# Kernel tuning notes

Measured on AMD Instinct MI355X. Metric: run time of the kernel, lower is better.

The kernel has to match this reference:

```python
import jax, jax.numpy as jnp
import numpy as np

B, NQ, NK, D, H = 2, 1024, 1024, 512, 32


def setup_inputs() -> dict:
    key = jax.random.key(0)
    ks = jax.random.split(key, 6)
    keys_t = jax.random.normal(ks[0], (B, NK, D), dtype=jnp.float32)
    queries = jax.random.normal(ks[1], (B, NQ, D), dtype=jnp.float32)
    # torch nn.Linear default init: U(-1/sqrt(fan_in), 1/sqrt(fan_in))
    s1 = 1.0 / np.sqrt(2 * D)
    W1 = jax.random.uniform(ks[2], (2 * D, H), jnp.float32, -s1, s1)  # (2d, hidden)
    b1 = jax.random.uniform(ks[3], (H,), jnp.float32, -s1, s1)
    s2 = 1.0 / np.sqrt(H)
    W2 = jax.random.uniform(ks[4], (H, 1), jnp.float32, -s2, s2)
    b2 = jax.random.uniform(ks[5], (1,), jnp.float32, -s2, s2)
    return {"keys": keys_t, "queries": queries, "W1": W1, "b1": b1, "W2": W2, "b2": b2}


def reference(keys, queries, W1, b1, W2, b2):
    # logits[b,q,k] = W2 . tanh(W1 @ cat(keys[b,k], queries[b,q]) + b1) + b2
    # Decompose first linear: cat(k,q) @ W1 == k @ W1[:D] + q @ W1[D:]
    d = keys.shape[-1]
    hk = jnp.einsum('bkd,dh->bkh', keys, W1[:d])      # (B, NK, H)
    hq = jnp.einsum('bqd,dh->bqh', queries, W1[d:])   # (B, NQ, H)
    h = jnp.tanh(hk[:, None, :, :] + hq[:, :, None, :] + b1)  # (B, NQ, NK, H)
    logits = jnp.einsum('bqkh,ho->bqko', h, W2)[..., 0] + b2[0]  # (B, NQ, NK)
    return logits
```

## Files before the change

kernel.cpp:

```cpp
#include <hip/hip_runtime.h>
#include <hip/hip_bf16.h>

#define NB 2
#define NQS 1024
#define NKS 1024
#define DD 512
#define HH 32
#define NKROW (NB * NKS)

typedef __attribute__((ext_vector_type(8))) short bf16x8;
typedef __attribute__((ext_vector_type(4))) float f32x4;

static __device__ __forceinline__ float fexp2(float x) {
#if __has_builtin(__builtin_amdgcn_exp2f)
  return __builtin_amdgcn_exp2f(x);
#else
  float r; asm("v_exp_f32 %0, %1" : "=v"(r) : "v"(x)); return r;
#endif
}
static __device__ __forceinline__ float frcp(float x) {
#if __has_builtin(__builtin_amdgcn_rcpf)
  return __builtin_amdgcn_rcpf(x);
#else
  float r; asm("v_rcp_f32 %0, %1" : "=v"(r) : "v"(x)); return r;
#endif
}

__global__ __launch_bounds__(64) void p1_proj_mfma(
    const float* __restrict__ keys, const float* __restrict__ queries,
    const float* __restrict__ W1, const float* __restrict__ b1,
    float* __restrict__ E) {
  const float S = 2.8853900817779268f;
  const int l = threadIdx.x;
  const int row0 = blockIdx.x * 16;
  const bool isq = row0 >= NKROW;
  const float* src = isq ? (queries + (size_t)(row0 - NKROW) * DD)
                         : (keys + (size_t)row0 * DD);
  const float* w1 = W1 + (isq ? (size_t)DD * HH : (size_t)0);
  const int m = l & 15, kq = l >> 4;
  f32x4 acc0 = {0.f, 0.f, 0.f, 0.f}, acc1 = {0.f, 0.f, 0.f, 0.f};
  const float* arow = src + (size_t)m * DD + kq * 8;
#pragma unroll 2
  for (int s = 0; s < 16; ++s) {
    const int kb = s * 32 + kq * 8;
    float4 a0 = *(const float4*)(arow + s * 32);
    float4 a1 = *(const float4*)(arow + s * 32 + 4);
    union { bf16x8 v; __hip_bfloat16 e[8]; } af, bf0, bf1;
    af.e[0] = __float2bfloat16(a0.x); af.e[1] = __float2bfloat16(a0.y);
    af.e[2] = __float2bfloat16(a0.z); af.e[3] = __float2bfloat16(a0.w);
    af.e[4] = __float2bfloat16(a1.x); af.e[5] = __float2bfloat16(a1.y);
    af.e[6] = __float2bfloat16(a1.z); af.e[7] = __float2bfloat16(a1.w);
    const float* wk = w1 + (size_t)kb * HH;
#pragma unroll
    for (int j = 0; j < 8; ++j) {
      bf0.e[j] = __float2bfloat16(wk[j * HH + m]);
      bf1.e[j] = __float2bfloat16(wk[j * HH + 16 + m]);
    }
    acc0 = __builtin_amdgcn_mfma_f32_16x16x32_bf16(af.v, bf0.v, acc0, 0, 0, 0);
    acc1 = __builtin_amdgcn_mfma_f32_16x16x32_bf16(af.v, bf1.v, acc1, 0, 0, 0);
  }
  float bias0 = 0.f, bias1 = 0.f;
  if (isq) { bias0 = b1[m]; bias1 = b1[16 + m]; }
#pragma unroll
  for (int r = 0; r < 4; ++r) {
    const int rr = row0 + kq * 4 + r;
    E[(size_t)rr * HH + m]      = fexp2(S * (acc0[r] + bias0));
    E[(size_t)rr * HH + 16 + m] = fexp2(S * (acc1[r] + bias1));
  }
}

__global__ __launch_bounds__(256) void p2_score(
    const float* __restrict__ E, const float* __restrict__ W2,
    const float* __restrict__ b2, float* __restrict__ out) {
  __shared__ float EkL[64 * 33];
  __shared__ float EqL[32 * 32];
  const int tid = threadIdx.x;
  const int k0 = blockIdx.x * 64, q0 = blockIdx.y * 32, b = blockIdx.z;
  const float* Ek_g = E + (size_t)(b * NKS + k0) * HH;
  const float* Eq_g = E + (size_t)NKROW * HH + (size_t)(b * NQS + q0) * HH;
  {
    int i = tid * 4;
    float4 w = *(const float4*)(Ek_g + i);
    int r = i >> 5, c = i & 31;
    EkL[r * 33 + c + 0] = w.x; EkL[r * 33 + c + 1] = w.y;
    EkL[r * 33 + c + 2] = w.z; EkL[r * 33 + c + 3] = w.w;
    i += 1024;
    w = *(const float4*)(Ek_g + i);
    r = i >> 5; c = i & 31;
    EkL[r * 33 + c + 0] = w.x; EkL[r * 33 + c + 1] = w.y;
    EkL[r * 33 + c + 2] = w.z; EkL[r * 33 + c + 3] = w.w;
    *(float4*)(EqL + tid * 4) = *(const float4*)(Eq_g + tid * 4);
  }
  float c0 = b2[0];
  float w2v[HH];
#pragma unroll
  for (int h = 0; h < HH; ++h) { float w = W2[h]; c0 += w; w2v[h] = -2.f * w; }
  float C01[16];
#pragma unroll
  for (int i = 0; i < 16; ++i) C01[i] = w2v[2 * i] + w2v[2 * i + 1];
  __syncthreads();
  const int kl = tid & 63, qg = tid >> 6;
  float ek[HH];
#pragma unroll
  for (int h = 0; h < HH; ++h) ek[h] = EkL[kl * 33 + h];
  float Aa[16], Bb[16];
#pragma unroll
  for (int i = 0; i < 16; ++i) {
    Aa[i] = w2v[2 * i] * ek[2 * i + 1];
    Bb[i] = w2v[2 * i + 1] * ek[2 * i];
  }
  float* outp = out + (size_t)(b * NQS + q0 + qg * 8) * NKS + k0 + kl;
  const float* eqrow = EqL + qg * 8 * HH;
#pragma unroll 2
  for (int j = 0; j < 8; ++j) {
    float acc0 = c0, acc1 = 0.f;
    const float4* e4 = (const float4*)(eqrow + (size_t)j * HH);
#pragma unroll
    for (int i2 = 0; i2 < 8; ++i2) {
      float4 ev = e4[i2];
      {
        const int i = 2 * i2;
        float da = fmaf(ek[2 * i], ev.x, 1.f);
        float db = fmaf(ek[2 * i + 1], ev.y, 1.f);
        float num = fmaf(Aa[i], ev.y, fmaf(Bb[i], ev.x, C01[i]));
        acc0 = fmaf(num, frcp(da * db), acc0);
      }
      {
        const int i = 2 * i2 + 1;
        float da = fmaf(ek[2 * i], ev.z, 1.f);
        float db = fmaf(ek[2 * i + 1], ev.w, 1.f);
        float num = fmaf(Aa[i], ev.w, fmaf(Bb[i], ev.z, C01[i]));
        acc1 = fmaf(num, frcp(da * db), acc1);
      }
    }
    outp[(size_t)j * NKS] = acc0 + acc1;
  }
}

extern "C" void kernel_launch(void* const* d_in, const int* in_sizes, int n_in,
                              void* d_out, int out_size, void* d_ws, size_t ws_size,
                              hipStream_t stream) {
  const float* keys = (const float*)d_in[0];
  const float* queries = (const float*)d_in[1];
  const float* W1 = (const float*)d_in[2];
  const float* b1 = (const float*)d_in[3];
  const float* W2 = (const float*)d_in[4];
  const float* b2 = (const float*)d_in[5];
  float* out = (float*)d_out;
  float* ws = (float*)d_ws;

  hipLaunchKernelGGL(p1_proj_mfma, dim3(256), dim3(64), 0, stream,
                     keys, queries, W1, b1, ws);
  hipLaunchKernelGGL(p2_score, dim3(NKS / 64, NQS / 32, NB), dim3(256), 0, stream,
                     ws, W2, b2, out);
}
```

Before: 22.92 us.

## Split projection K across four waves with LDS-staged W1; drop LDS staging in score kernel

The projection kernel now uses 256 threads per block. W1 is converted to bf16 once into LDS, and the 512-long reduction is split across four waves, which combine their partial accumulators through shared memory before the exp2 epilogue. This is meant to add parallelism and stop each wave from re-reading and re-converting W1 from global memory, at the cost of a full W1 staging pass per block plus two barriers. The score kernel drops its LDS staging and barrier: each thread loads its key row directly into registers, and the query rows, now wave-uniform through readfirstlane, are read straight from global memory and rely on cache and scalar or broadcast loads.

```diff
diff --git a/kernel.cpp b/kernel.cpp
--- a/kernel.cpp
+++ b/kernel.cpp
@@ -7,6 +7,7 @@
 #define DD 512
 #define HH 32
 #define NKROW (NB * NKS)
+#define W1S 34
 
 typedef __attribute__((ext_vector_type(8))) short bf16x8;
 typedef __attribute__((ext_vector_type(4))) float f32x4;
@@ -26,98 +27,104 @@
 #endif
 }
 
-__global__ __launch_bounds__(64) void p1_proj_mfma(
+__global__ __launch_bounds__(256) void p1_proj_mfma(
     const float* __restrict__ keys, const float* __restrict__ queries,
     const float* __restrict__ W1, const float* __restrict__ b1,
     float* __restrict__ E) {
+  __shared__ __hip_bfloat16 W1L[DD * W1S];
+  __shared__ float red[4 * 2 * 64 * 4];
   const float S = 2.8853900817779268f;
-  const int l = threadIdx.x;
+  const int tid = threadIdx.x;
   const int row0 = blockIdx.x * 16;
   const bool isq = row0 >= NKROW;
-  const float* src = isq ? (queries + (size_t)(row0 - NKROW) * DD)
-                         : (keys + (size_t)row0 * DD);
-  const float* w1 = W1 + (isq ? (size_t)DD * HH : (size_t)0);
+  const float* src = isq ? queries + (size_t)(row0 - NKROW) * DD
+                         : keys + (size_t)row0 * DD;
+  const float* w1 = W1 + (isq ? (size_t)DD * HH : 0);
+#pragma unroll
+  for (int s = 0; s < 16; ++s) {
+    const int f = tid + s * 256;
+    float4 v = *(const float4*)(w1 + (size_t)f * 4);
+    const int k = f >> 3, h0 = (f & 7) * 4;
+    __hip_bfloat16* p = &W1L[k * W1S + h0];
+    p[0] = __float2bfloat16(v.x); p[1] = __float2bfloat16(v.y);
+    p[2] = __float2bfloat16(v.z); p[3] = __float2bfloat16(v.w);
+  }
+  __syncthreads();
+  const int l = tid & 63, w = tid >> 6;
   const int m = l & 15, kq = l >> 4;
   f32x4 acc0 = {0.f, 0.f, 0.f, 0.f}, acc1 = {0.f, 0.f, 0.f, 0.f};
-  const float* arow = src + (size_t)m * DD + kq * 8;
-#pragma unroll 2
-  for (int s = 0; s < 16; ++s) {
-    const int kb = s * 32 + kq * 8;
+  const float* arow = src + (size_t)m * DD + w * 128 + kq * 8;
+  union Frag { bf16x8 v; __hip_bfloat16 e[8]; };
+#pragma unroll
+  for (int s = 0; s < 4; ++s) {
+    const int kb = w * 128 + s * 32;
     float4 a0 = *(const float4*)(arow + s * 32);
     float4 a1 = *(const float4*)(arow + s * 32 + 4);
-    union { bf16x8 v; __hip_bfloat16 e[8]; } af, bf0, bf1;
+    Frag af, bf0, bf1;
     af.e[0] = __float2bfloat16(a0.x); af.e[1] = __float2bfloat16(a0.y);
     af.e[2] = __float2bfloat16(a0.z); af.e[3] = __float2bfloat16(a0.w);
     af.e[4] = __float2bfloat16(a1.x); af.e[5] = __float2bfloat16(a1.y);
     af.e[6] = __float2bfloat16(a1.z); af.e[7] = __float2bfloat16(a1.w);
-    const float* wk = w1 + (size_t)kb * HH;
+    const __hip_bfloat16* bp = &W1L[(kb + kq * 8) * W1S + m];
 #pragma unroll
     for (int j = 0; j < 8; ++j) {
-      bf0.e[j] = __float2bfloat16(wk[j * HH + m]);
-      bf1.e[j] = __float2bfloat16(wk[j * HH + 16 + m]);
+      bf0.e[j] = bp[j * W1S];
+      bf1.e[j] = bp[j * W1S + 16];
     }
     acc0 = __builtin_amdgcn_mfma_f32_16x16x32_bf16(af.v, bf0.v, acc0, 0, 0, 0);
     acc1 = __builtin_amdgcn_mfma_f32_16x16x32_bf16(af.v, bf1.v, acc1, 0, 0, 0);
   }
-  float bias0 = 0.f, bias1 = 0.f;
-  if (isq) { bias0 = b1[m]; bias1 = b1[16 + m]; }
+  *(f32x4*)(&red[((w * 2 + 0) * 64 + l) * 4]) = acc0;
+  *(f32x4*)(&red[((w * 2 + 1) * 64 + l) * 4]) = acc1;
+  __syncthreads();
 #pragma unroll
-  for (int r = 0; r < 4; ++r) {
-    const int rr = row0 + kq * 4 + r;
-    E[(size_t)rr * HH + m]      = fexp2(S * (acc0[r] + bias0));
-    E[(size_t)rr * HH + 16 + m] = fexp2(S * (acc1[r] + bias1));
+  for (int u = 0; u < 2; ++u) {
+    const int o = tid + u * 256;
+    const int rr = o >> 5, h = o & 31;
+    const int t = h >> 4, mm = h & 15;
+    const int ll = ((rr >> 2) << 4) | mm, r = rr & 3;
+    float sum = red[(0 + t) * 256 + ll * 4 + r] + red[(2 + t) * 256 + ll * 4 + r] +
+                red[(4 + t) * 256 + ll * 4 + r] + red[(6 + t) * 256 + ll * 4 + r];
+    if (isq) sum += b1[h];
+    E[(size_t)(row0 + rr) * HH + h] = fexp2(S * sum);
   }
 }
 
 __global__ __launch_bounds__(256) void p2_score(
     const float* __restrict__ E, const float* __restrict__ W2,
     const float* __restrict__ b2, float* __restrict__ out) {
-  __shared__ float EkL[64 * 33];
-  __shared__ float EqL[32 * 32];
   const int tid = threadIdx.x;
+  const int kl = tid & 63;
+  const int qg = __builtin_amdgcn_readfirstlane(tid >> 6);
   const int k0 = blockIdx.x * 64, q0 = blockIdx.y * 32, b = blockIdx.z;
-  const float* Ek_g = E + (size_t)(b * NKS + k0) * HH;
-  const float* Eq_g = E + (size_t)NKROW * HH + (size_t)(b * NQS + q0) * HH;
-  {
-    int i = tid * 4;
-    float4 w = *(const float4*)(Ek_g + i);
-    int r = i >> 5, c = i & 31;
-    EkL[r * 33 + c + 0] = w.x; EkL[r * 33 + c + 1] = w.y;
-    EkL[r * 33 + c + 2] = w.z; EkL[r * 33 + c + 3] = w.w;
-    i += 1024;
-    w = *(const float4*)(Ek_g + i);
-    r = i >> 5; c = i & 31;
-    EkL[r * 33 + c + 0] = w.x; EkL[r * 33 + c + 1] = w.y;
-    EkL[r * 33 + c + 2] = w.z; EkL[r * 33 + c + 3] = w.w;
-    *(float4*)(EqL + tid * 4) = *(const float4*)(Eq_g + tid * 4);
+  const float* ekp = E + (size_t)(b * NKS + k0 + kl) * HH;
+  float ek[HH];
+#pragma unroll
+  for (int i = 0; i < 8; ++i) {
+    float4 v = *(const float4*)(ekp + i * 4);
+    ek[i * 4 + 0] = v.x; ek[i * 4 + 1] = v.y;
+    ek[i * 4 + 2] = v.z; ek[i * 4 + 3] = v.w;
   }
   float c0 = b2[0];
   float w2v[HH];
 #pragma unroll
-  for (int h = 0; h < HH; ++h) { float w = W2[h]; c0 += w; w2v[h] = -2.f * w; }
-  float C01[16];
-#pragma unroll
-  for (int i = 0; i < 16; ++i) C01[i] = w2v[2 * i] + w2v[2 * i + 1];
-  __syncthreads();
-  const int kl = tid & 63, qg = tid >> 6;
-  float ek[HH];
-#pragma unroll
-  for (int h = 0; h < HH; ++h) ek[h] = EkL[kl * 33 + h];
-  float Aa[16], Bb[16];
+  for (int h = 0; h < HH; ++h) { float ww = W2[h]; c0 += ww; w2v[h] = -2.f * ww; }
+  float Aa[16], Bb[16], C01[16];
 #pragma unroll
   for (int i = 0; i < 16; ++i) {
     Aa[i] = w2v[2 * i] * ek[2 * i + 1];
     Bb[i] = w2v[2 * i + 1] * ek[2 * i];
+    C01[i] = w2v[2 * i] + w2v[2 * i + 1];
   }
-  float* outp = out + (size_t)(b * NQS + q0 + qg * 8) * NKS + k0 + kl;
-  const float* eqrow = EqL + qg * 8 * HH;
+  const float* eqb = E + ((size_t)NKROW + (size_t)b * NQS + q0 + qg * 8) * HH;
+  float* outp = out + ((size_t)b * NQS + q0 + qg * 8) * NKS + k0 + kl;
 #pragma unroll 2
   for (int j = 0; j < 8; ++j) {
+    const float* ej = eqb + (size_t)j * HH;
     float acc0 = c0, acc1 = 0.f;
-    const float4* e4 = (const float4*)(eqrow + (size_t)j * HH);
 #pragma unroll
     for (int i2 = 0; i2 < 8; ++i2) {
-      float4 ev = e4[i2];
+      float4 ev = *(const float4*)(ej + i2 * 4);
       {
         const int i = 2 * i2;
         float da = fmaf(ek[2 * i], ev.x, 1.f);
@@ -149,7 +156,7 @@
   float* out = (float*)d_out;
   float* ws = (float*)d_ws;
 
-  hipLaunchKernelGGL(p1_proj_mfma, dim3(256), dim3(64), 0, stream,
+  hipLaunchKernelGGL(p1_proj_mfma, dim3(256), dim3(256), 0, stream,
                      keys, queries, W1, b1, ws);
   hipLaunchKernelGGL(p2_score, dim3(NKS / 64, NQS / 32, NB), dim3(256), 0, stream,
                      ws, W2, b2, out);
```

Measured after the change: 21.18 us. 7.6% less time.
